# Kernel optimization log

Hardware: AMD Instinct MI355X
Metric: run time of the kernel (lower is better)

## Reference

```python
import jax, jax.numpy as jnp
import numpy as np

SIZE = 10000
PADDING_IDX = -1
SMOOTHING = 0.1
CONFIDENCE = 1.0 - SMOOTHING
NORMALIZE_LENGTH = False
NUM_EXPERTS = 8
LB_COEF = 0.01
Z_COEF = 0.001


def setup_inputs() -> dict:
    key = jax.random.key(0)
    ks = jax.random.split(key, 8)
    B, T, V, K, E = 8, 1024, SIZE, 2, NUM_EXPERTS
    N = B * T
    return {
        "x": jax.random.normal(ks[0], (B, T, V), dtype=jnp.float32),
        "target": jax.random.randint(ks[1], (B, T), 0, V, dtype=jnp.int64),
        "topk_values_local": jax.random.uniform(ks[2], (N, K), dtype=jnp.float32),
        "topk_indices_local": jax.random.randint(ks[3], (N, K), 0, E, dtype=jnp.int64),
        "gate_logits_local": jax.random.normal(ks[4], (N, E), dtype=jnp.float32),
        "topk_values_global": jax.random.uniform(ks[5], (N, K), dtype=jnp.float32),
        "topk_indices_global": jax.random.randint(ks[6], (N, K), 0, E, dtype=jnp.int64),
        "gate_logits_global": jax.random.normal(ks[7], (N, E), dtype=jnp.float32),
    }


def _load_balance(topk_values, topk_indices):
    # Single-pass histogram + segment-sum (replaces the per-expert python loop).
    idx = topk_indices.reshape(-1)
    vals = topk_values.reshape(-1)
    expert_loads = jax.ops.segment_sum(jnp.ones_like(vals), idx, num_segments=NUM_EXPERTS)
    logits_sum = jax.ops.segment_sum(vals, idx, num_segments=NUM_EXPERTS)
    num_tokens = topk_values.size / topk_values.shape[-1]
    return NUM_EXPERTS / num_tokens * jnp.sum(expert_loads * logits_sum)


def _z_loss(gate_logits):
    return jnp.mean(jnp.square(jax.nn.logsumexp(gate_logits, axis=-1)))


def reference(x, target, topk_values_local, topk_indices_local, gate_logits_local,
              topk_values_global, topk_indices_global, gate_logits_global):
    B = x.shape[0]
    x2 = x.reshape(-1, SIZE)              # (N, V)
    tgt = target.reshape(-1)              # (N,)
    ignore = tgt == PADDING_IDX
    total = tgt.shape[0] - jnp.sum(ignore)
    tgt = jnp.where(ignore, 0, tgt)

    smooth = SMOOTHING / (SIZE - 1)
    logp = jax.nn.log_softmax(x2, axis=-1)
    logp_tgt = jnp.take_along_axis(logp, tgt[:, None], axis=-1)[:, 0]
    # KLDiv(reduction='none') summed over classes, per row:
    #   sum_j td_j*log(td_j) - sum_j td_j*logp_j
    ent = (SIZE - 1) * smooth * np.log(smooth) + CONFIDENCE * np.log(CONFIDENCE)
    cross = smooth * (jnp.sum(logp, axis=-1) - logp_tgt) + CONFIDENCE * logp_tgt
    kl_row = jnp.where(ignore, 0.0, ent - cross)
    denom = jnp.where(NORMALIZE_LENGTH, total, B).astype(x.dtype)
    label_smoothing_loss = jnp.sum(kl_row) / denom

    load_loss_local = _load_balance(topk_values_local, topk_indices_local)
    load_loss_global = _load_balance(topk_values_global, topk_indices_global)
    z_local = _z_loss(gate_logits_local)
    z_global = _z_loss(gate_logits_global)

    return (label_smoothing_loss
            + LB_COEF * (load_loss_local + load_loss_global) / 2
            + Z_COEF * (z_local + z_global) / 2)
```

## Files before the change

### kernel.cpp

```cpp
#include <hip/hip_runtime.h>
#include <math.h>

#define VDIM 10000
#define NROWS 8192
#define NEXP 8
#define KTOP 2
#define NB_LS NROWS
#define NB_Z 64
#define NB_LB 2
#define BLOCK 256

__global__ void zero_out_kernel(float* out) {
    if (threadIdx.x == 0) out[0] = 0.0f;
}

__global__ __launch_bounds__(BLOCK) void fused_loss(
    const float* __restrict__ x, const int* __restrict__ target,
    const float* __restrict__ tv_l, const int* __restrict__ ti_l,
    const float* __restrict__ gl_l,
    const float* __restrict__ tv_g, const int* __restrict__ ti_g,
    const float* __restrict__ gl_g,
    float* __restrict__ out)
{
    __shared__ float sh[96];
    const int bid  = blockIdx.x;
    const int tid  = threadIdx.x;
    const int lane = tid & 63;
    const int wave = tid >> 6;

    if (bid < NB_LS) {
        const float4* xr = (const float4*)(x + (size_t)bid * VDIM);
        float s = 0.f, t = 0.f;
        for (int i = tid; i < VDIM / 4; i += BLOCK) {
            float4 v = xr[i];
            t += v.x + v.y + v.z + v.w;
            s += __expf(v.x) + __expf(v.y) + __expf(v.z) + __expf(v.w);
        }
        #pragma unroll
        for (int off = 32; off > 0; off >>= 1) {
            s += __shfl_down(s, off);
            t += __shfl_down(t, off);
        }
        if (lane == 0) { sh[wave] = s; sh[8 + wave] = t; }
        __syncthreads();
        if (tid == 0) {
            float S = sh[0] + sh[1] + sh[2] + sh[3];
            float T = sh[8] + sh[9] + sh[10] + sh[11];
            int tg = target[bid];
            if (tg != -1) {
                float lse      = logf(S);
                float xt       = x[(size_t)bid * VDIM + tg];
                float logp_tgt = xt - lse;
                float sum_logp = T - (float)VDIM * lse;
                const float SMOOTH = 0.1f / 9999.0f;
                const float CONF   = 0.9f;
                const float ENT    = -1.2461070100920437f;
                float cross = SMOOTH * (sum_logp - logp_tgt) + CONF * logp_tgt;
                float kl = ENT - cross;
                atomicAdd(out, kl * 0.125f);
            }
        }
    } else if (bid < NB_LS + NB_Z) {
        int item = (bid - NB_LS) * BLOCK + tid;
        int side = item >> 13;
        int row  = item & (NROWS - 1);
        const float4* g = (const float4*)((side ? gl_g : gl_l) + (size_t)row * NEXP);
        float4 a = g[0], b = g[1];
        float s = __expf(a.x) + __expf(a.y) + __expf(a.z) + __expf(a.w)
                + __expf(b.x) + __expf(b.y) + __expf(b.z) + __expf(b.w);
        float lse = logf(s);
        float z = lse * lse;
        #pragma unroll
        for (int off = 32; off > 0; off >>= 1) z += __shfl_down(z, off);
        if (lane == 0) sh[wave] = z;
        __syncthreads();
        if (tid == 0) {
            float Z = sh[0] + sh[1] + sh[2] + sh[3];
            atomicAdd(out, Z * 6.103515625e-08f);
        }
    } else {
        int side = bid - NB_LS - NB_Z;
        const float* tv = side ? tv_g : tv_l;
        const int*   ti = side ? ti_g : ti_l;
        float cnt[NEXP], sm[NEXP];
        #pragma unroll
        for (int j = 0; j < NEXP; ++j) { cnt[j] = 0.f; sm[j] = 0.f; }
        for (int i = tid; i < NROWS * KTOP; i += BLOCK) {
            int e = ti[i];
            float v = tv[i];
            #pragma unroll
            for (int j = 0; j < NEXP; ++j) {
                if (e == j) { cnt[j] += 1.f; sm[j] += v; }
            }
        }
        #pragma unroll
        for (int j = 0; j < NEXP; ++j) {
            #pragma unroll
            for (int off = 32; off > 0; off >>= 1) {
                cnt[j] += __shfl_down(cnt[j], off);
                sm[j]  += __shfl_down(sm[j], off);
            }
        }
        if (lane == 0) {
            #pragma unroll
            for (int j = 0; j < NEXP; ++j) {
                sh[wave * 16 + j]     = cnt[j];
                sh[wave * 16 + 8 + j] = sm[j];
            }
        }
        __syncthreads();
        if (tid == 0) {
            float dot = 0.f;
            #pragma unroll
            for (int j = 0; j < NEXP; ++j) {
                float c  = sh[j]     + sh[16 + j] + sh[32 + j] + sh[48 + j];
                float ss = sh[8 + j] + sh[24 + j] + sh[40 + j] + sh[56 + j];
                dot += c * ss;
            }
            atomicAdd(out, dot * 4.8828125e-06f);
        }
    }
}

extern "C" void kernel_launch(void* const* d_in, const int* in_sizes, int n_in,
                              void* d_out, int out_size, void* d_ws, size_t ws_size,
                              hipStream_t stream) {
    const float* x    = (const float*)d_in[0];
    const int*   tgt  = (const int*)d_in[1];
    const float* tv_l = (const float*)d_in[2];
    const int*   ti_l = (const int*)d_in[3];
    const float* gl_l = (const float*)d_in[4];
    const float* tv_g = (const float*)d_in[5];
    const int*   ti_g = (const int*)d_in[6];
    const float* gl_g = (const float*)d_in[7];
    float* out = (float*)d_out;

    zero_out_kernel<<<1, 64, 0, stream>>>(out);
    fused_loss<<<NB_LS + NB_Z + NB_LB, BLOCK, 0, stream>>>(
        x, tgt, tv_l, ti_l, gl_l, tv_g, ti_g, gl_g, out);
}
```

Before: 476.0 us.

## Issue all row loads up front with nontemporal loads and replace atomics with two-stage reduction

Measured after the change: 439.5 us. 7.7% less time.

```diff
diff --git a/kernel.cpp b/kernel.cpp
--- a/kernel.cpp
+++ b/kernel.cpp
@@ -8,11 +8,10 @@
 #define NB_LS NROWS
 #define NB_Z 64
 #define NB_LB 2
+#define NB_TOTAL (NB_LS + NB_Z + NB_LB)
 #define BLOCK 256
 
-__global__ void zero_out_kernel(float* out) {
-    if (threadIdx.x == 0) out[0] = 0.0f;
-}
+typedef float f4 __attribute__((ext_vector_type(4)));
 
 __global__ __launch_bounds__(BLOCK) void fused_loss(
     const float* __restrict__ x, const int* __restrict__ target,
@@ -20,22 +19,33 @@
     const float* __restrict__ gl_l,
     const float* __restrict__ tv_g, const int* __restrict__ ti_g,
     const float* __restrict__ gl_g,
-    float* __restrict__ out)
+    float* __restrict__ ws)
 {
-    __shared__ float sh[96];
+    __shared__ float sh[128];
     const int bid  = blockIdx.x;
     const int tid  = threadIdx.x;
     const int lane = tid & 63;
     const int wave = tid >> 6;
 
     if (bid < NB_LS) {
-        const float4* xr = (const float4*)(x + (size_t)bid * VDIM);
+        const f4* xr = (const f4*)(x + (size_t)bid * VDIM);
+        f4 v[9];
+        #pragma unroll
+        for (int i = 0; i < 9; ++i)
+            v[i] = __builtin_nontemporal_load(&xr[tid + i * BLOCK]);
+        f4 vt = {0.f, 0.f, 0.f, 0.f};
+        if (tid < 2500 - 9 * BLOCK)
+            vt = __builtin_nontemporal_load(&xr[tid + 9 * BLOCK]);
         float s = 0.f, t = 0.f;
-        for (int i = tid; i < VDIM / 4; i += BLOCK) {
-            float4 v = xr[i];
-            t += v.x + v.y + v.z + v.w;
-            s += __expf(v.x) + __expf(v.y) + __expf(v.z) + __expf(v.w);
+        #pragma unroll
+        for (int i = 0; i < 9; ++i) {
+            t += v[i].x + v[i].y + v[i].z + v[i].w;
+            s += __expf(v[i].x) + __expf(v[i].y) + __expf(v[i].z) + __expf(v[i].w);
         }
+        t += vt.x + vt.y + vt.z + vt.w;
+        if (tid < 2500 - 9 * BLOCK)
+            s += __expf(vt.x) + __expf(vt.y) + __expf(vt.z) + __expf(vt.w);
+
         #pragma unroll
         for (int off = 32; off > 0; off >>= 1) {
             s += __shfl_down(s, off);
@@ -47,6 +57,7 @@
             float S = sh[0] + sh[1] + sh[2] + sh[3];
             float T = sh[8] + sh[9] + sh[10] + sh[11];
             int tg = target[bid];
+            float r = 0.f;
             if (tg != -1) {
                 float lse      = logf(S);
                 float xt       = x[(size_t)bid * VDIM + tg];
@@ -56,16 +67,16 @@
                 const float CONF   = 0.9f;
                 const float ENT    = -1.2461070100920437f;
                 float cross = SMOOTH * (sum_logp - logp_tgt) + CONF * logp_tgt;
-                float kl = ENT - cross;
-                atomicAdd(out, kl * 0.125f);
+                r = (ENT - cross) * 0.125f;
             }
+            ws[bid] = r;
         }
     } else if (bid < NB_LS + NB_Z) {
         int item = (bid - NB_LS) * BLOCK + tid;
         int side = item >> 13;
         int row  = item & (NROWS - 1);
-        const float4* g = (const float4*)((side ? gl_g : gl_l) + (size_t)row * NEXP);
-        float4 a = g[0], b = g[1];
+        const f4* g = (const f4*)((side ? gl_g : gl_l) + (size_t)row * NEXP);
+        f4 a = g[0], b = g[1];
         float s = __expf(a.x) + __expf(a.y) + __expf(a.z) + __expf(a.w)
                 + __expf(b.x) + __expf(b.y) + __expf(b.z) + __expf(b.w);
         float lse = logf(s);
@@ -76,7 +87,7 @@
         __syncthreads();
         if (tid == 0) {
             float Z = sh[0] + sh[1] + sh[2] + sh[3];
-            atomicAdd(out, Z * 6.103515625e-08f);
+            ws[bid] = Z * 6.103515625e-08f;
         }
     } else {
         int side = bid - NB_LS - NB_Z;
@@ -117,8 +128,29 @@
                 float ss = sh[8 + j] + sh[24 + j] + sh[40 + j] + sh[56 + j];
                 dot += c * ss;
             }
-            atomicAdd(out, dot * 4.8828125e-06f);
+            ws[bid] = dot * 4.8828125e-06f;
         }
+    }
+}
+
+__global__ __launch_bounds__(1024) void final_reduce(
+    const float* __restrict__ ws, float* __restrict__ out)
+{
+    __shared__ float sh[16];
+    const int tid  = threadIdx.x;
+    const int lane = tid & 63;
+    const int wave = tid >> 6;
+    float s = 0.f;
+    for (int i = tid; i < NB_TOTAL; i += 1024) s += ws[i];
+    #pragma unroll
+    for (int off = 32; off > 0; off >>= 1) s += __shfl_down(s, off);
+    if (lane == 0) sh[wave] = s;
+    __syncthreads();
+    if (tid == 0) {
+        float tot = 0.f;
+        #pragma unroll
+        for (int w = 0; w < 16; ++w) tot += sh[w];
+        out[0] = tot;
     }
 }
 
@@ -133,9 +165,10 @@
     const float* tv_g = (const float*)d_in[5];
     const int*   ti_g = (const int*)d_in[6];
     const float* gl_g = (const float*)d_in[7];
+    float* ws  = (float*)d_ws;
     float* out = (float*)d_out;
 
-    zero_out_kernel<<<1, 64, 0, stream>>>(out);
-    fused_loss<<<NB_LS + NB_Z + NB_LB, BLOCK, 0, stream>>>(
-        x, tgt, tv_l, ti_l, gl_l, tv_g, ti_g, gl_g, out);
+    fused_loss<<<NB_TOTAL, BLOCK, 0, stream>>>(
+        x, tgt, tv_l, ti_l, gl_l, tv_g, ti_g, gl_g, ws);
+    final_reduce<<<1, 1024, 0, stream>>>(ws, out);
 }
```
